# Optimization experiments

Measured on AMD Instinct MI355X. Metric: run time of the kernel, lower is better.

## Reference

```python
import jax, jax.numpy as jnp
import numpy as np

MD_R = 64          # low-rank R
NMF_STEPS = 7      # EVAL_STEPS
INV_T = 1.0
EPS = 1e-6
GN_GROUPS = 32


def _nmf_step(x, bases, coef):
    # x: (B,D,N), bases: (B,D,R), coef: (B,N,R) -- multiplicative NMF updates
    btb = jnp.einsum('bdr,bdk->brk', bases, bases)                 # (B,R,R)
    coef = coef * jnp.einsum('bdn,bdr->bnr', x, bases) / (
        jnp.einsum('bnr,brk->bnk', coef, btb) + EPS)
    ctc = jnp.einsum('bnr,bnk->brk', coef, coef)                   # (B,R,R)
    bases = bases * jnp.einsum('bdn,bnr->bdr', x, coef) / (
        jnp.einsum('bdr,brk->bdk', bases, ctc) + EPS)
    return bases, coef


def setup_inputs() -> dict:
    key = jax.random.key(0)
    ks = jax.random.split(key, 7)
    B, C, H, W = 8, 256, 64, 64
    x = jax.random.normal(ks[0], (B, C, H, W), jnp.float32)
    w_in = jax.random.normal(ks[1], (C, C), jnp.float32) * 0.02
    b_in = jnp.zeros((C,), jnp.float32)
    w_out = jax.random.normal(ks[2], (C, C), jnp.float32) * 0.02
    gn_gamma = jnp.ones((C,), jnp.float32)
    gn_beta = jnp.zeros((C,), jnp.float32)
    bases_init = jax.random.uniform(ks[3], (B, C, MD_R), jnp.float32)  # RAND_INIT bases
    return {"x": x, "w_in": w_in, "b_in": b_in, "w_out": w_out,
            "gn_gamma": gn_gamma, "gn_beta": gn_beta, "bases_init": bases_init}


def reference(x, w_in, b_in, w_out, gn_gamma, gn_beta, bases_init):
    B, C, H, W = x.shape
    N = H * W
    # ham_in: 1x1 conv with bias, then relu
    h = jnp.einsum('bchw,oc->bohw', x, w_in) + b_in[None, :, None, None]
    h = jax.nn.relu(h)
    # NMF2D: flatten spatial (SPATIAL=True, S=1 -> D=C)
    xm = h.reshape(B, C, N)                                         # (B,D,N)
    # F.normalize(rand bases, dim=1)
    bases = bases_init / jnp.maximum(
        jnp.linalg.norm(bases_init, axis=1, keepdims=True), 1e-12)
    # local_inference runs under no_grad in the original; math identical here
    xs = jax.lax.stop_gradient(xm)
    coef = jax.nn.softmax(INV_T * jnp.einsum('bdn,bdr->bnr', xs, bases), axis=-1)
    for _ in range(NMF_STEPS):
        bases, coef = _nmf_step(xs, bases, coef)
    bases = jax.lax.stop_gradient(bases)
    coef = jax.lax.stop_gradient(coef)
    # compute_coef (differentiable w.r.t. xm)
    btb = jnp.einsum('bdr,bdk->brk', bases, bases)
    coef = coef * jnp.einsum('bdn,bdr->bnr', xm, bases) / (
        jnp.einsum('bnr,brk->bnk', coef, btb) + EPS)
    rec = jnp.einsum('bdr,bnr->bdn', bases, coef).reshape(B, C, H, W)
    # ham_out: 1x1 conv (no bias) + GroupNorm(32)
    o = jnp.einsum('bchw,oc->bohw', rec, w_out)
    g = o.reshape(B, GN_GROUPS, C // GN_GROUPS, H, W)
    mu = g.mean(axis=(2, 3, 4), keepdims=True)
    var = g.var(axis=(2, 3, 4), keepdims=True)
    g = (g - mu) * jax.lax.rsqrt(var + 1e-5)
    o = g.reshape(B, C, H, W) * gn_gamma[None, :, None, None] + gn_beta[None, :, None, None]
    # residual + relu
    return jax.nn.relu(x + o)
```

## Files before the change

### kernel.cpp

```cpp
#include <hip/hip_runtime.h>

#define B_ 8
#define C_ 256
#define N_ 4096
#define R_ 64
#define STEPS_ 7
#define NCH_ 128
#define NSP_ 32
#define EPS_ 1e-6f

typedef unsigned short u16;
typedef short bf8v __attribute__((ext_vector_type(8)));
typedef float f4v __attribute__((ext_vector_type(4)));

#define MFMA(a, b, c) __builtin_amdgcn_mfma_f32_16x16x32_bf16((a), (b), (c), 0, 0, 0)

__device__ __forceinline__ u16 bf(float x) {
  union { float f; unsigned u; } v; v.f = x;
  return (u16)((v.u + 0x7FFFu + ((v.u >> 16) & 1u)) >> 16);
}
__device__ __forceinline__ float bf2f(u16 x) {
  union { unsigned u; float f; } v; v.u = (unsigned)x << 16; return v.f;
}
__device__ __forceinline__ bf8v ldf(const u16* p) { return *(const bf8v*)p; }

__global__ __launch_bounds__(256)
void prep_kernel(const float* __restrict__ binit, float* __restrict__ bases,
                 u16* __restrict__ basesT,
                 const float* __restrict__ w1, const float* __restrict__ w2,
                 u16* __restrict__ w1b, u16* __restrict__ w2b) {
  const int t = threadIdx.x;
  if (blockIdx.x >= 8) {
    const int i = (blockIdx.x - 8) * 256 + t;
    w1b[i] = bf(w1[i]);
    w2b[i] = bf(w2[i]);
    return;
  }
  const int b = blockIdx.x;
  const int rr = t & 63, dq = t >> 6;
  const float* src = binit + (size_t)b * C_ * R_;
  float* dst = bases + (size_t)b * C_ * R_;
  u16* dT  = basesT + (size_t)b * R_ * C_;
  float vals[64];
  float s = 0.f;
#pragma unroll
  for (int i = 0; i < 64; ++i) {
    float v = src[(size_t)(dq + 4 * i) * R_ + rr];
    vals[i] = v; s = fmaf(v, v, s);
  }
  __shared__ float red[4][64];
  red[dq][rr] = s;
  __syncthreads();
  float nrm = fmaxf(sqrtf(red[0][rr] + red[1][rr] + red[2][rr] + red[3][rr]), 1e-12f);
  const float inv = 1.f / nrm;
#pragma unroll
  for (int i = 0; i < 64; ++i) {
    const int d = dq + 4 * i;
    const float v = vals[i] * inv;
    dst[(size_t)d * R_ + rr] = v;
    dT[(size_t)rr * C_ + d]  = bf(v);
  }
}

__global__ __launch_bounds__(256)
void conv1_kernel(const float* __restrict__ x, const u16* __restrict__ W,
                  const float* __restrict__ bias, u16* __restrict__ h_dn,
                  u16* __restrict__ h_nd) {
  const int nb0 = blockIdx.x * 128, ob0 = blockIdx.y * 128, b = blockIdx.z;
  const int t = threadIdx.x, w = t >> 6, lane = t & 63, g = lane >> 4, c = lane & 15;
  const int nloc = (w >> 1) * 64, o_base = ob0 + (w & 1) * 64;
  const float* xb = x + (size_t)b * C_ * N_ + nb0;
  __shared__ u16 xa_s[128][40];
  __shared__ float lds[64][65];
  const int skk = t >> 3, sn = (t & 7) * 16;
  f4v acc[4][4] = {};
  for (int k0 = 0; k0 < C_; k0 += 32) {
    if (k0) __syncthreads();
    const float* src = &xb[(size_t)(k0 + skk) * N_ + sn];
    float4 v0 = *(const float4*)src;
    float4 v1 = *(const float4*)(src + 4);
    float4 v2 = *(const float4*)(src + 8);
    float4 v3 = *(const float4*)(src + 12);
    xa_s[sn + 0][skk] = bf(v0.x);  xa_s[sn + 1][skk] = bf(v0.y);
    xa_s[sn + 2][skk] = bf(v0.z);  xa_s[sn + 3][skk] = bf(v0.w);
    xa_s[sn + 4][skk] = bf(v1.x);  xa_s[sn + 5][skk] = bf(v1.y);
    xa_s[sn + 6][skk] = bf(v1.z);  xa_s[sn + 7][skk] = bf(v1.w);
    xa_s[sn + 8][skk] = bf(v2.x);  xa_s[sn + 9][skk] = bf(v2.y);
    xa_s[sn + 10][skk] = bf(v2.z); xa_s[sn + 11][skk] = bf(v2.w);
    xa_s[sn + 12][skk] = bf(v3.x); xa_s[sn + 13][skk] = bf(v3.y);
    xa_s[sn + 14][skk] = bf(v3.z); xa_s[sn + 15][skk] = bf(v3.w);
    __syncthreads();
    bf8v av[4], wv[4];
#pragma unroll
    for (int mi = 0; mi < 4; ++mi)
      av[mi] = *(const bf8v*)&xa_s[nloc + mi * 16 + c][g * 8];
#pragma unroll
    for (int nj = 0; nj < 4; ++nj)
      wv[nj] = ldf(W + (size_t)(o_base + nj * 16 + c) * C_ + k0 + g * 8);
#pragma unroll
    for (int mi = 0; mi < 4; ++mi)
#pragma unroll
      for (int nj = 0; nj < 4; ++nj)
        acc[mi][nj] = MFMA(av[mi], wv[nj], acc[mi][nj]);
  }
  __syncthreads();
  for (int p = 0; p < 4; ++p) {
    if (w == p) {
#pragma unroll
      for (int mi = 0; mi < 4; ++mi)
#pragma unroll
        for (int nj = 0; nj < 4; ++nj) {
          const float bb = bias[o_base + nj * 16 + c];
#pragma unroll
          for (int rg = 0; rg < 4; ++rg)
            lds[mi * 16 + g * 4 + rg][nj * 16 + c] = fmaxf(acc[mi][nj][rg] + bb, 0.f);
        }
    }
    __syncthreads();
    const int pn = nb0 + (p >> 1) * 64, po = ob0 + (p & 1) * 64;
    {
      const int n = t >> 2, ob2 = (t & 3) * 16;
      __align__(16) u16 tmp[16];
#pragma unroll
      for (int j = 0; j < 16; ++j) tmp[j] = bf(lds[n][ob2 + j]);
      u16* o = h_nd + (size_t)b * N_ * C_ + (size_t)(pn + n) * C_ + po + ob2;
      *(uint4*)o = *(uint4*)tmp; *(uint4*)(o + 8) = *(uint4*)(tmp + 8);
    }
    {
      const int oo = t >> 2, nb2 = (t & 3) * 16;
      __align__(16) u16 tmp[16];
#pragma unroll
      for (int j = 0; j < 16; ++j) tmp[j] = bf(lds[nb2 + j][oo]);
      u16* o = h_dn + (size_t)b * C_ * N_ + (size_t)(po + oo) * N_ + pn + nb2;
      *(uint4*)o = *(uint4*)tmp; *(uint4*)(o + 8) = *(uint4*)(tmp + 8);
    }
    __syncthreads();
  }
}

template<int MODE>
__global__ __launch_bounds__(512)
void nmf_kernel(const u16* __restrict__ h_nd, const u16* __restrict__ h_dn,
                const u16* __restrict__ basesT, const u16* __restrict__ w2b,
                u16* __restrict__ coef_bf, u16* __restrict__ m2_bf,
                float* __restrict__ ctcp, u16* __restrict__ xcp) {
  const int nc0 = blockIdx.x * NCH_;
  const int b = blockIdx.y;
  const int t = threadIdx.x, w = t >> 6, lane = t & 63, g = lane >> 4, c = lane & 15;
  __shared__ u16 bT_s[64 * 256];
  __shared__ u16 btb_s[64][72];
  __shared__ u16 coef_s[128][72];
  __shared__ u16 coefT_s[64][136];
  const u16* hb = h_nd + (size_t)b * N_ * C_;
  const u16* bT = basesT + (size_t)b * R_ * C_;
  u16* cb = coef_bf + (size_t)b * N_ * R_;

#pragma unroll
  for (int i = 0; i < 4; ++i) {
    const int lin = t + i * 512;
    const int r = lin >> 5, k = lin & 31;
    *(uint4*)&bT_s[r * 256 + ((k ^ (r & 7)) * 8)] =
        *(const uint4*)&bT[(size_t)r * C_ + k * 8];
  }
  if (MODE != 0) {
    const int row = t >> 2, seg = (t & 3) * 16;
    const u16* src = cb + (size_t)(nc0 + row) * R_ + seg;
    *(uint4*)&coef_s[row][seg] = *(const uint4*)src;
    *(uint4*)&coef_s[row][seg + 8] = *(const uint4*)(src + 8);
  }
  __syncthreads();

  const int nl = w * 16 + c;

  f4v num[4] = {}, bt[4] = {};
  const u16* An = hb + (size_t)(nc0 + nl) * C_;
  for (int k0 = 0; k0 < C_; k0 += 32) {
    const int kc = (k0 >> 3) + g;
    bf8v bv[4];
#pragma unroll
    for (int nj = 0; nj < 4; ++nj)
      bv[nj] = *(const bf8v*)&bT_s[(nj * 16 + c) * 256 + ((kc ^ (c & 7)) * 8)];
    bf8v a = ldf(An + k0 + g * 8);
#pragma unroll
    for (int nj = 0; nj < 4; ++nj) num[nj] = MFMA(a, bv[nj], num[nj]);
    if (w < 4) {
      bf8v a2 = *(const bf8v*)&bT_s[(w * 16 + c) * 256 + ((kc ^ (c & 7)) * 8)];
#pragma unroll
      for (int nj = 0; nj < 4; ++nj) bt[nj] = MFMA(a2, bv[nj], bt[nj]);
    }
  }

  if (MODE == 0) {
#pragma unroll
    for (int rg = 0; rg < 4; ++rg) {
      float m = fmaxf(fmaxf(num[0][rg], num[1][rg]), fmaxf(num[2][rg], num[3][rg]));
#pragma unroll
      for (int off = 1; off < 16; off <<= 1) m = fmaxf(m, __shfl_xor(m, off));
      float e[4], s = 0.f;
#pragma unroll
      for (int nj = 0; nj < 4; ++nj) { e[nj] = __expf(num[nj][rg] - m); s += e[nj]; }
#pragma unroll
      for (int off = 1; off < 16; off <<= 1) s += __shfl_xor(s, off);
      const float inv = 1.f / s;
#pragma unroll
      for (int nj = 0; nj < 4; ++nj)
        coef_s[w * 16 + g * 4 + rg][nj * 16 + c] = bf(e[nj] * inv);
    }
  }

  if (w < 4) {
#pragma unroll
    for (int nj = 0; nj < 4; ++nj)
#pragma unroll
      for (int rg = 0; rg < 4; ++rg)
        btb_s[w * 16 + g * 4 + rg][nj * 16 + c] = bf(bt[nj][rg]);
  }
  __syncthreads();

  f4v den[4] = {};
#pragma unroll
  for (int k0 = 0; k0 < R_; k0 += 32) {
    bf8v a = *(const bf8v*)&coef_s[nl][k0 + g * 8];
#pragma unroll
    for (int nj = 0; nj < 4; ++nj)
      den[nj] = MFMA(a, *(const bf8v*)&btb_s[nj * 16 + c][k0 + g * 8], den[nj]);
  }
  __syncthreads();

#pragma unroll
  for (int nj = 0; nj < 4; ++nj)
#pragma unroll
    for (int rg = 0; rg < 4; ++rg) {
      const int row = w * 16 + g * 4 + rg, r = nj * 16 + c;
      const float old = bf2f(coef_s[row][r]);
      const u16 nv = bf(old * num[nj][rg] / (den[nj][rg] + EPS_));
      coef_s[row][r] = nv;
      if (MODE <= 1) coefT_s[r][row] = nv;
    }
  __syncthreads();

  {
    const int row = t >> 2, seg = (t & 3) * 16;
    u16* dst = cb + (size_t)(nc0 + row) * R_ + seg;
    *(uint4*)dst = *(const uint4*)&coef_s[row][seg];
    *(uint4*)(dst + 8) = *(const uint4*)&coef_s[row][seg + 8];
  }

  if (MODE <= 1) {
    f4v xa[2][4] = {};
    const u16* hd = h_dn + (size_t)b * C_ * N_;
    for (int k0 = 0; k0 < NCH_; k0 += 32) {
      bf8v bv[4];
#pragma unroll
      for (int nj = 0; nj < 4; ++nj)
        bv[nj] = *(const bf8v*)&coefT_s[nj * 16 + c][k0 + g * 8];
#pragma unroll
      for (int mi = 0; mi < 2; ++mi) {
        bf8v a = ldf(hd + (size_t)(w * 32 + mi * 16 + c) * N_ + nc0 + k0 + g * 8);
#pragma unroll
        for (int nj = 0; nj < 4; ++nj) xa[mi][nj] = MFMA(a, bv[nj], xa[mi][nj]);
      }
    }
    u16* xo = xcp + ((size_t)b * NSP_ + blockIdx.x) * (C_ * R_);
#pragma unroll
    for (int mi = 0; mi < 2; ++mi)
#pragma unroll
      for (int nj = 0; nj < 4; ++nj)
#pragma unroll
        for (int rg = 0; rg < 4; ++rg)
          xo[(size_t)(w * 32 + mi * 16 + g * 4 + rg) * R_ + nj * 16 + c] = bf(xa[mi][nj][rg]);
    if (w < 4) {
      f4v ca[4] = {};
      for (int k0 = 0; k0 < NCH_; k0 += 32) {
        bf8v a = *(const bf8v*)&coefT_s[w * 16 + c][k0 + g * 8];
#pragma unroll
        for (int nj = 0; nj < 4; ++nj)
          ca[nj] = MFMA(a, *(const bf8v*)&coefT_s[nj * 16 + c][k0 + g * 8], ca[nj]);
      }
      float* co = ctcp + ((size_t)b * NSP_ + blockIdx.x) * (R_ * R_);
#pragma unroll
      for (int nj = 0; nj < 4; ++nj)
#pragma unroll
        for (int rg = 0; rg < 4; ++rg)
          co[(size_t)(w * 16 + g * 4 + rg) * R_ + nj * 16 + c] = ca[nj][rg];
    }
  }

  if (MODE == 2 && blockIdx.x == 0) {
    f4v ma[2][4] = {};
    for (int k0 = 0; k0 < C_; k0 += 32) {
      const int kc = (k0 >> 3) + g;
      bf8v bv[4];
#pragma unroll
      for (int nj = 0; nj < 4; ++nj)
        bv[nj] = *(const bf8v*)&bT_s[(nj * 16 + c) * 256 + ((kc ^ (c & 7)) * 8)];
#pragma unroll
      for (int mi = 0; mi < 2; ++mi) {
        bf8v a = ldf(w2b + (size_t)(w * 32 + mi * 16 + c) * C_ + k0 + g * 8);
#pragma unroll
        for (int nj = 0; nj < 4; ++nj) ma[mi][nj] = MFMA(a, bv[nj], ma[mi][nj]);
      }
    }
    u16* mo = m2_bf + (size_t)b * C_ * R_;
#pragma unroll
    for (int mi = 0; mi < 2; ++mi)
#pragma unroll
      for (int nj = 0; nj < 4; ++nj)
#pragma unroll
        for (int rg = 0; rg < 4; ++rg)
          mo[(size_t)(w * 32 + mi * 16 + g * 4 + rg) * R_ + nj * 16 + c] = bf(ma[mi][nj][rg]);
  }
}

__global__ __launch_bounds__(256)
void bases_update_kernel(const u16* __restrict__ xcp, const float* __restrict__ ctcp,
                         float* __restrict__ bases, u16* __restrict__ basesT) {
  const int dt = blockIdx.x & 3, rt = blockIdx.x >> 2, b = blockIdx.y;
  const int d0 = dt * 64, rb = rt * 16;
  float* bb = bases + (size_t)b * C_ * R_;
  __shared__ float ctc_s[64][16];
  __shared__ float b_s[64][65];
  const int t = threadIdx.x;
  {
    const int k = t >> 2, cr = (t & 3) * 4;
    float4 a = make_float4(0, 0, 0, 0);
    for (int s = 0; s < NSP_; ++s) {
      float4 v = *(const float4*)&ctcp[((size_t)b * NSP_ + s) * (R_ * R_) + (size_t)k * R_ + rb + cr];
      a.x += v.x; a.y += v.y; a.z += v.z; a.w += v.w;
    }
    *(float4*)&ctc_s[k][cr] = a;
  }
  {
    const int lc = t & 63, lr = t >> 6;
#pragma unroll
    for (int p = 0; p < 16; ++p)
      b_s[lr + 4 * p][lc] = bb[(size_t)(d0 + lr + 4 * p) * R_ + lc];
  }
  __syncthreads();
  const int dd = t >> 2, r0 = rb + (t & 3) * 4, cr = (t & 3) * 4;
  float4 num2 = make_float4(0, 0, 0, 0);
  for (int s = 0; s < NSP_; ++s) {
    ushort4 v = *(const ushort4*)&xcp[(((size_t)b * NSP_ + s) * C_ + d0 + dd) * R_ + r0];
    num2.x += bf2f(v.x); num2.y += bf2f(v.y);
    num2.z += bf2f(v.z); num2.w += bf2f(v.w);
  }
  float4 den = make_float4(0, 0, 0, 0);
#pragma unroll
  for (int k = 0; k < 64; ++k) {
    const float a = b_s[dd][k];
    float4 cv = *(const float4*)&ctc_s[k][cr];
    den.x = fmaf(a, cv.x, den.x); den.y = fmaf(a, cv.y, den.y);
    den.z = fmaf(a, cv.z, den.z); den.w = fmaf(a, cv.w, den.w);
  }
  float4 o;
  o.x = b_s[dd][r0 + 0] * num2.x / (den.x + EPS_);
  o.y = b_s[dd][r0 + 1] * num2.y / (den.y + EPS_);
  o.z = b_s[dd][r0 + 2] * num2.z / (den.z + EPS_);
  o.w = b_s[dd][r0 + 3] * num2.w / (den.w + EPS_);
  *(float4*)&bb[(size_t)(d0 + dd) * R_ + r0] = o;
  u16* oT = basesT + (size_t)b * R_ * C_ + d0 + dd;
  oT[(size_t)(r0 + 0) * C_] = bf(o.x); oT[(size_t)(r0 + 1) * C_] = bf(o.y);
  oT[(size_t)(r0 + 2) * C_] = bf(o.z); oT[(size_t)(r0 + 3) * C_] = bf(o.w);
}

__global__ __launch_bounds__(256)
void conv2_kernel(const u16* __restrict__ coef, const u16* __restrict__ m2,
                  float* __restrict__ of32, float* __restrict__ pstats) {
  const int nb0 = blockIdx.x * 128, ob0 = blockIdx.y * 128, b = blockIdx.z;
  const int t = threadIdx.x, w = t >> 6, lane = t & 63, g = lane >> 4, c = lane & 15;
  const int n_base = nb0 + (w >> 1) * 64, o_base = ob0 + (w & 1) * 64;
  const u16* Ab = coef + (size_t)b * N_ * R_;
  const u16* Wb = m2 + (size_t)b * C_ * R_;
  f4v acc[4][4] = {};
#pragma unroll
  for (int k0 = 0; k0 < R_; k0 += 32) {
    bf8v av[4], wv[4];
#pragma unroll
    for (int mi = 0; mi < 4; ++mi)
      av[mi] = ldf(Ab + (size_t)(n_base + mi * 16 + c) * R_ + k0 + g * 8);
#pragma unroll
    for (int nj = 0; nj < 4; ++nj)
      wv[nj] = ldf(Wb + (size_t)(o_base + nj * 16 + c) * R_ + k0 + g * 8);
#pragma unroll
    for (int mi = 0; mi < 4; ++mi)
#pragma unroll
      for (int nj = 0; nj < 4; ++nj)
        acc[mi][nj] = MFMA(av[mi], wv[nj], acc[mi][nj]);
  }
  __shared__ float lds[64][65];
  float sacc0 = 0.f, sacc1 = 0.f, s2acc0 = 0.f, s2acc1 = 0.f;
  for (int p = 0; p < 4; ++p) {
    if (w == p) {
#pragma unroll
      for (int mi = 0; mi < 4; ++mi)
#pragma unroll
        for (int nj = 0; nj < 4; ++nj)
#pragma unroll
          for (int rg = 0; rg < 4; ++rg)
            lds[mi * 16 + g * 4 + rg][nj * 16 + c] = acc[mi][nj][rg];
    }
    __syncthreads();
    const int pn = nb0 + (p >> 1) * 64, po = ob0 + (p & 1) * 64;
    const int oo = t >> 2, nb2 = (t & 3) * 16;
    float* o = of32 + (size_t)b * C_ * N_ + (size_t)(po + oo) * N_ + pn + nb2;
    float ls = 0.f, ls2 = 0.f;
#pragma unroll
    for (int q = 0; q < 4; ++q) {
      float4 v = make_float4(lds[nb2 + q * 4 + 0][oo], lds[nb2 + q * 4 + 1][oo],
                             lds[nb2 + q * 4 + 2][oo], lds[nb2 + q * 4 + 3][oo]);
      *(float4*)&o[q * 4] = v;
      ls += v.x + v.y + v.z + v.w;
      ls2 = fmaf(v.x, v.x, ls2); ls2 = fmaf(v.y, v.y, ls2);
      ls2 = fmaf(v.z, v.z, ls2); ls2 = fmaf(v.w, v.w, ls2);
    }
    if ((p & 1) == 0) { sacc0 += ls; s2acc0 += ls2; }
    else              { sacc1 += ls; s2acc1 += ls2; }
    __syncthreads();
  }
  {
    const int oo = t >> 2, q4 = t & 3;
    lds[oo][q4] = sacc0;      lds[oo][4 + q4] = s2acc0;
    lds[oo][8 + q4] = sacc1;  lds[oo][12 + q4] = s2acc1;
    __syncthreads();
    if (t < 128) {
      const int hh = t >> 6, oo2 = t & 63;
      const int base = hh * 8;
      float s = lds[oo2][base] + lds[oo2][base + 1] + lds[oo2][base + 2] + lds[oo2][base + 3];
      float s2 = lds[oo2][base + 4] + lds[oo2][base + 5] + lds[oo2][base + 6] + lds[oo2][base + 7];
      float* ps = pstats + (((size_t)blockIdx.z * 32 + blockIdx.x) * 256 +
                            (size_t)blockIdx.y * 128 + hh * 64 + oo2) * 2;
      ps[0] = s; ps[1] = s2;
    }
  }
}

__global__ __launch_bounds__(256)
void gn_final_kernel(const float* __restrict__ x, const float* __restrict__ gamma,
                     const float* __restrict__ beta, const float* __restrict__ pstats,
                     float* __restrict__ out) {
  const int t = threadIdx.x;
  const size_t gid0 = (size_t)blockIdx.x * 256;
  const size_t idx0 = gid0 * 4;
  const int b = (int)(idx0 >> 20);
  const int c = (int)((idx0 & ((1u << 20) - 1)) >> 12);
  const int g = c >> 3;
  float s, s2;
  {
    const int nb = t >> 3, ch = g * 8 + (t & 7);
    const float* ps = pstats + (((size_t)b * 32 + nb) * 256 + ch) * 2;
    s = ps[0]; s2 = ps[1];
  }
#pragma unroll
  for (int off = 32; off > 0; off >>= 1) { s += __shfl_down(s, off); s2 += __shfl_down(s2, off); }
  __shared__ float rs[4], rs2[4], fin[2];
  if ((t & 63) == 0) { rs[t >> 6] = s; rs2[t >> 6] = s2; }
  __syncthreads();
  if (t == 0) {
    float S = rs[0] + rs[1] + rs[2] + rs[3];
    float S2 = rs2[0] + rs2[1] + rs2[2] + rs2[3];
    float mean = S / 32768.f;
    float var = S2 / 32768.f - mean * mean;
    fin[0] = mean; fin[1] = rsqrtf(var + 1e-5f);
  }
  __syncthreads();
  const float mean = fin[0], rstd = fin[1];
  const float ga = gamma[c] * rstd;
  const float be = beta[c] - mean * ga;
  const size_t gid = gid0 + t;
  float4 ov = ((const float4*)out)[gid];
  float4 xv = ((const float4*)x)[gid];
  float4 r;
  r.x = fmaxf(fmaf(ov.x, ga, be) + xv.x, 0.f);
  r.y = fmaxf(fmaf(ov.y, ga, be) + xv.y, 0.f);
  r.z = fmaxf(fmaf(ov.z, ga, be) + xv.z, 0.f);
  r.w = fmaxf(fmaf(ov.w, ga, be) + xv.w, 0.f);
  ((float4*)out)[gid] = r;
}

extern "C" void kernel_launch(void* const* d_in, const int* in_sizes, int n_in,
                              void* d_out, int out_size, void* d_ws, size_t ws_size,
                              hipStream_t stream) {
  (void)in_sizes; (void)n_in; (void)out_size; (void)ws_size;
  const float* x     = (const float*)d_in[0];
  const float* w_in  = (const float*)d_in[1];
  const float* b_in  = (const float*)d_in[2];
  const float* w_out = (const float*)d_in[3];
  const float* gamma = (const float*)d_in[4];
  const float* beta  = (const float*)d_in[5];
  const float* binit = (const float*)d_in[6];
  float* out = (float*)d_out;

  float* p = (float*)d_ws;
  u16* h_nd = (u16*)p;      p += 4194304;
  u16* h_dn = (u16*)p;      p += 4194304;
  u16* coef_bf = (u16*)p;   p += 1048576;
  float* bases = p;         p += 131072;
  u16* basesT = (u16*)p;    p += 65536;
  u16* m2_bf = (u16*)p;     p += 65536;
  float* ctcp = p;          p += 1048576;
  u16* xcp = (u16*)p;       p += 2097152;
  u16* w1b = (u16*)p;       p += 32768;
  u16* w2b = (u16*)p;       p += 32768;
  float* pstats = p;        p += 131072;

  prep_kernel<<<dim3(264), 256, 0, stream>>>(binit, bases, basesT, w_in, w_out, w1b, w2b);
  conv1_kernel<<<dim3(32, 2, 8), 256, 0, stream>>>(x, w1b, b_in, h_dn, h_nd);

  nmf_kernel<0><<<dim3(32, 8), 512, 0, stream>>>(h_nd, h_dn, basesT, w2b, coef_bf,
                                                 m2_bf, ctcp, xcp);
  bases_update_kernel<<<dim3(16, 8), 256, 0, stream>>>(xcp, ctcp, bases, basesT);
  for (int it = 1; it < STEPS_; ++it) {
    nmf_kernel<1><<<dim3(32, 8), 512, 0, stream>>>(h_nd, h_dn, basesT, w2b, coef_bf,
                                                   m2_bf, ctcp, xcp);
    bases_update_kernel<<<dim3(16, 8), 256, 0, stream>>>(xcp, ctcp, bases, basesT);
  }
  nmf_kernel<2><<<dim3(32, 8), 512, 0, stream>>>(h_nd, h_dn, basesT, w2b, coef_bf,
                                                 m2_bf, ctcp, xcp);
  conv2_kernel<<<dim3(32, 2, 8), 256, 0, stream>>>(coef_bf, m2_bf, out, pstats);
  gn_final_kernel<<<dim3((B_ * C_ * N_) / 4 / 256), 256, 0, stream>>>(x, gamma, beta,
                                                                      pstats, out);
}
```

Baseline: 254.1 us.

## Halve NMF spatial chunk, split waves between num and BtB, prefetch h fragments

Result: slower. 305.5 us (+20.2%).

```diff
diff --git a/kernel.cpp b/kernel.cpp
--- a/kernel.cpp
+++ b/kernel.cpp
@@ -5,8 +5,8 @@
 #define N_ 4096
 #define R_ 64
 #define STEPS_ 7
-#define NCH_ 128
-#define NSP_ 32
+#define NCH_ 64
+#define NSP_ 64
 #define EPS_ 1e-6f
 
 typedef unsigned short u16;
@@ -139,7 +139,7 @@
 }
 
 template<int MODE>
-__global__ __launch_bounds__(512)
+__global__ __launch_bounds__(512, 4)
 void nmf_kernel(const u16* __restrict__ h_nd, const u16* __restrict__ h_dn,
                 const u16* __restrict__ basesT, const u16* __restrict__ w2b,
                 u16* __restrict__ coef_bf, u16* __restrict__ m2_bf,
@@ -149,11 +149,21 @@
   const int t = threadIdx.x, w = t >> 6, lane = t & 63, g = lane >> 4, c = lane & 15;
   __shared__ u16 bT_s[64 * 256];
   __shared__ u16 btb_s[64][72];
-  __shared__ u16 coef_s[128][72];
-  __shared__ u16 coefT_s[64][136];
+  __shared__ u16 coef_s[64][72];
+  __shared__ u16 coefT_s[64][72];
   const u16* hb = h_nd + (size_t)b * N_ * C_;
+  const u16* hd = h_dn + (size_t)b * C_ * N_;
   const u16* bT = basesT + (size_t)b * R_ * C_;
   u16* cb = coef_bf + (size_t)b * N_ * R_;
+
+  bf8v hfr[2][2];
+  if (MODE <= 1) {
+#pragma unroll
+    for (int kk = 0; kk < 2; ++kk)
+#pragma unroll
+      for (int mi = 0; mi < 2; ++mi)
+        hfr[kk][mi] = ldf(hd + (size_t)(w * 32 + mi * 16 + c) * N_ + nc0 + kk * 32 + g * 8);
+  }
 
 #pragma unroll
   for (int i = 0; i < 4; ++i) {
@@ -163,103 +173,107 @@
         *(const uint4*)&bT[(size_t)r * C_ + k * 8];
   }
   if (MODE != 0) {
-    const int row = t >> 2, seg = (t & 3) * 16;
-    const u16* src = cb + (size_t)(nc0 + row) * R_ + seg;
-    *(uint4*)&coef_s[row][seg] = *(const uint4*)src;
-    *(uint4*)&coef_s[row][seg + 8] = *(const uint4*)(src + 8);
-  }
-  __syncthreads();
-
-  const int nl = w * 16 + c;
-
-  f4v num[4] = {}, bt[4] = {};
-  const u16* An = hb + (size_t)(nc0 + nl) * C_;
-  for (int k0 = 0; k0 < C_; k0 += 32) {
-    const int kc = (k0 >> 3) + g;
-    bf8v bv[4];
+    const int row = t >> 3, seg = (t & 7) * 8;
+    *(uint4*)&coef_s[row][seg] = *(const uint4*)&cb[(size_t)(nc0 + row) * R_ + seg];
+  }
+  __syncthreads();
+
+  f4v num[4] = {};
+  if (w < 4) {
+    const u16* An = hb + (size_t)(nc0 + w * 16 + c) * C_;
+    for (int k0 = 0; k0 < C_; k0 += 32) {
+      const int kc = (k0 >> 3) + g;
+      bf8v bv[4];
+#pragma unroll
+      for (int nj = 0; nj < 4; ++nj)
+        bv[nj] = *(const bf8v*)&bT_s[(nj * 16 + c) * 256 + ((kc ^ (c & 7)) * 8)];
+      bf8v a = ldf(An + k0 + g * 8);
+#pragma unroll
+      for (int nj = 0; nj < 4; ++nj) num[nj] = MFMA(a, bv[nj], num[nj]);
+    }
+    if (MODE == 0) {
+#pragma unroll
+      for (int rg = 0; rg < 4; ++rg) {
+        float m = fmaxf(fmaxf(num[0][rg], num[1][rg]), fmaxf(num[2][rg], num[3][rg]));
+#pragma unroll
+        for (int off = 1; off < 16; off <<= 1) m = fmaxf(m, __shfl_xor(m, off));
+        float e[4], s = 0.f;
+#pragma unroll
+        for (int nj = 0; nj < 4; ++nj) { e[nj] = __expf(num[nj][rg] - m); s += e[nj]; }
+#pragma unroll
+        for (int off = 1; off < 16; off <<= 1) s += __shfl_xor(s, off);
+        const float inv = 1.f / s;
+#pragma unroll
+        for (int nj = 0; nj < 4; ++nj)
+          coef_s[w * 16 + g * 4 + rg][nj * 16 + c] = bf(e[nj] * inv);
+      }
+    }
+  } else {
+    f4v bt[4] = {};
+    const int rr = (w - 4) * 16 + c;
+    for (int k0 = 0; k0 < C_; k0 += 32) {
+      const int kc = (k0 >> 3) + g;
+      bf8v bv[4];
+#pragma unroll
+      for (int nj = 0; nj < 4; ++nj)
+        bv[nj] = *(const bf8v*)&bT_s[(nj * 16 + c) * 256 + ((kc ^ (c & 7)) * 8)];
+      bf8v a2 = *(const bf8v*)&bT_s[rr * 256 + ((kc ^ (c & 7)) * 8)];
+#pragma unroll
+      for (int nj = 0; nj < 4; ++nj) bt[nj] = MFMA(a2, bv[nj], bt[nj]);
+    }
 #pragma unroll
     for (int nj = 0; nj < 4; ++nj)
-      bv[nj] = *(const bf8v*)&bT_s[(nj * 16 + c) * 256 + ((kc ^ (c & 7)) * 8)];
-    bf8v a = ldf(An + k0 + g * 8);
-#pragma unroll
-    for (int nj = 0; nj < 4; ++nj) num[nj] = MFMA(a, bv[nj], num[nj]);
-    if (w < 4) {
-      bf8v a2 = *(const bf8v*)&bT_s[(w * 16 + c) * 256 + ((kc ^ (c & 7)) * 8)];
-#pragma unroll
-      for (int nj = 0; nj < 4; ++nj) bt[nj] = MFMA(a2, bv[nj], bt[nj]);
-    }
-  }
-
-  if (MODE == 0) {
-#pragma unroll
-    for (int rg = 0; rg < 4; ++rg) {
-      float m = fmaxf(fmaxf(num[0][rg], num[1][rg]), fmaxf(num[2][rg], num[3][rg]));
-#pragma unroll
-      for (int off = 1; off < 16; off <<= 1) m = fmaxf(m, __shfl_xor(m, off));
-      float e[4], s = 0.f;
-#pragma unroll
-      for (int nj = 0; nj < 4; ++nj) { e[nj] = __expf(num[nj][rg] - m); s += e[nj]; }
-#pragma unroll
-      for (int off = 1; off < 16; off <<= 1) s += __shfl_xor(s, off);
-      const float inv = 1.f / s;
-#pragma unroll
-      for (int nj = 0; nj < 4; ++nj)
-        coef_s[w * 16 + g * 4 + rg][nj * 16 + c] = bf(e[nj] * inv);
-    }
-  }
-
+#pragma unroll
+      for (int rg = 0; rg < 4; ++rg)
+        btb_s[(w - 4) * 16 + g * 4 + rg][nj * 16 + c] = bf(bt[nj][rg]);
+  }
+  __syncthreads();
+
+  f4v den[4] = {};
   if (w < 4) {
 #pragma unroll
+    for (int k0 = 0; k0 < R_; k0 += 32) {
+      bf8v a = *(const bf8v*)&coef_s[w * 16 + c][k0 + g * 8];
+#pragma unroll
+      for (int nj = 0; nj < 4; ++nj)
+        den[nj] = MFMA(a, *(const bf8v*)&btb_s[nj * 16 + c][k0 + g * 8], den[nj]);
+    }
+  }
+  __syncthreads();
+
+  if (w < 4) {
+#pragma unroll
     for (int nj = 0; nj < 4; ++nj)
 #pragma unroll
-      for (int rg = 0; rg < 4; ++rg)
-        btb_s[w * 16 + g * 4 + rg][nj * 16 + c] = bf(bt[nj][rg]);
-  }
-  __syncthreads();
-
-  f4v den[4] = {};
-#pragma unroll
-  for (int k0 = 0; k0 < R_; k0 += 32) {
-    bf8v a = *(const bf8v*)&coef_s[nl][k0 + g * 8];
-#pragma unroll
-    for (int nj = 0; nj < 4; ++nj)
-      den[nj] = MFMA(a, *(const bf8v*)&btb_s[nj * 16 + c][k0 + g * 8], den[nj]);
-  }
-  __syncthreads();
-
-#pragma unroll
-  for (int nj = 0; nj < 4; ++nj)
-#pragma unroll
-    for (int rg = 0; rg < 4; ++rg) {
-      const int row = w * 16 + g * 4 + rg, r = nj * 16 + c;
-      const float old = bf2f(coef_s[row][r]);
-      const u16 nv = bf(old * num[nj][rg] / (den[nj][rg] + EPS_));
-      coef_s[row][r] = nv;
-      if (MODE <= 1) coefT_s[r][row] = nv;
-    }
+      for (int rg = 0; rg < 4; ++rg) {
+        const int row = w * 16 + g * 4 + rg, r = nj * 16 + c;
+        const float old = bf2f(coef_s[row][r]);
+        const u16 nv = bf(old * num[nj][rg] / (den[nj][rg] + EPS_));
+        coef_s[row][r] = nv;
+        if (MODE <= 1) coefT_s[r][row] = nv;
+      }
+  }
   __syncthreads();
 
   {
-    const int row = t >> 2, seg = (t & 3) * 16;
-    u16* dst = cb + (size_t)(nc0 + row) * R_ + seg;
-    *(uint4*)dst = *(const uint4*)&coef_s[row][seg];
-    *(uint4*)(dst + 8) = *(const uint4*)&coef_s[row][seg + 8];
+    const int row = t >> 3, seg = (t & 7) * 8;
+    *(uint4*)&cb[(size_t)(nc0 + row) * R_ + seg] = *(const uint4*)&coef_s[row][seg];
   }
 
   if (MODE <= 1) {
     f4v xa[2][4] = {};
-    const u16* hd = h_dn + (size_t)b * C_ * N_;
-    for (int k0 = 0; k0 < NCH_; k0 += 32) {
+#pragma unroll
+    for (int kk = 0; kk < 2; ++kk) {
+      const int k0 = kk * 32;
       bf8v bv[4];
 #pragma unroll
       for (int nj = 0; nj < 4; ++nj)
         bv[nj] = *(const bf8v*)&coefT_s[nj * 16 + c][k0 + g * 8];
 #pragma unroll
-      for (int mi = 0; mi < 2; ++mi) {
-        bf8v a = ldf(hd + (size_t)(w * 32 + mi * 16 + c) * N_ + nc0 + k0 + g * 8);
-#pragma unroll
-        for (int nj = 0; nj < 4; ++nj) xa[mi][nj] = MFMA(a, bv[nj], xa[mi][nj]);
-      }
+      for (int mi = 0; mi < 2; ++mi)
+#pragma unroll
+        for (int nj = 0; nj < 4; ++nj)
+          xa[mi][nj] = MFMA(hfr[kk][mi], bv[nj], xa[mi][nj]);
     }
     u16* xo = xcp + ((size_t)b * NSP_ + blockIdx.x) * (C_ * R_);
 #pragma unroll
@@ -271,7 +285,8 @@
           xo[(size_t)(w * 32 + mi * 16 + g * 4 + rg) * R_ + nj * 16 + c] = bf(xa[mi][nj][rg]);
     if (w < 4) {
       f4v ca[4] = {};
-      for (int k0 = 0; k0 < NCH_; k0 += 32) {
+#pragma unroll
+      for (int k0 = 0; k0 < R_; k0 += 32) {
         bf8v a = *(const bf8v*)&coefT_s[w * 16 + c][k0 + g * 8];
 #pragma unroll
         for (int nj = 0; nj < 4; ++nj)
@@ -497,8 +512,8 @@
   float* bases = p;         p += 131072;
   u16* basesT = (u16*)p;    p += 65536;
   u16* m2_bf = (u16*)p;     p += 65536;
-  float* ctcp = p;          p += 1048576;
-  u16* xcp = (u16*)p;       p += 2097152;
+  float* ctcp = p;          p += 2097152;
+  u16* xcp = (u16*)p;       p += 4194304;
   u16* w1b = (u16*)p;       p += 32768;
   u16* w2b = (u16*)p;       p += 32768;
   float* pstats = p;        p += 131072;
@@ -506,16 +521,16 @@
   prep_kernel<<<dim3(264), 256, 0, stream>>>(binit, bases, basesT, w_in, w_out, w1b, w2b);
   conv1_kernel<<<dim3(32, 2, 8), 256, 0, stream>>>(x, w1b, b_in, h_dn, h_nd);
 
-  nmf_kernel<0><<<dim3(32, 8), 512, 0, stream>>>(h_nd, h_dn, basesT, w2b, coef_bf,
-                                                 m2_bf, ctcp, xcp);
+  nmf_kernel<0><<<dim3(NSP_, 8), 512, 0, stream>>>(h_nd, h_dn, basesT, w2b, coef_bf,
+                                                   m2_bf, ctcp, xcp);
   bases_update_kernel<<<dim3(16, 8), 256, 0, stream>>>(xcp, ctcp, bases, basesT);
   for (int it = 1; it < STEPS_; ++it) {
-    nmf_kernel<1><<<dim3(32, 8), 512, 0, stream>>>(h_nd, h_dn, basesT, w2b, coef_bf,
+    nmf_kernel<1><<<dim3(NSP_, 8), 512, 0, stream>>>(h_nd, h_dn, basesT, w2b, coef_bf,
+                                                     m2_bf, ctcp, xcp);
+    bases_update_kernel<<<dim3(16, 8), 256, 0, stream>>>(xcp, ctcp, bases, basesT);
+  }
+  nmf_kernel<2><<<dim3(NSP_, 8), 512, 0, stream>>>(h_nd, h_dn, basesT, w2b, coef_bf,
                                                    m2_bf, ctcp, xcp);
-    bases_update_kernel<<<dim3(16, 8), 256, 0, stream>>>(xcp, ctcp, bases, basesT);
-  }
-  nmf_kernel<2><<<dim3(32, 8), 512, 0, stream>>>(h_nd, h_dn, basesT, w2b, coef_bf,
-                                                 m2_bf, ctcp, xcp);
   conv2_kernel<<<dim3(32, 2, 8), 256, 0, stream>>>(coef_bf, m2_bf, out, pstats);
   gn_final_kernel<<<dim3((B_ * C_ * N_) / 4 / 256), 256, 0, stream>>>(x, gamma, beta,
                                                                       pstats, out);
```
